# Performance work log

Measured on AMD Instinct MI355X. Metric: run time of the kernel, lower is better.

## Reference

```python
import jax, jax.numpy as jnp
import numpy as np


def setup_inputs() -> dict:
    key = jax.random.key(0)
    k_y, k_cb = jax.random.split(key)
    B, C, H, W = 8, 192, 64, 64
    G, K = 8, 512
    d = C // G  # 24
    y = jax.random.normal(k_y, (B, C, H, W), dtype=jnp.float32)
    codebooks = jax.random.normal(k_cb, (G, K, d), dtype=jnp.float32)
    return {"y": y, "codebooks": codebooks}


def reference(y, codebooks):
    # y: [B, C, H, W]; codebooks: [G, K, d] with C == G*d
    B, C, H, W = y.shape
    G, K, d = codebooks.shape
    # split channels into G groups of dim d -> vectors at each spatial pos
    x = y.reshape(B, G, d, H, W).transpose(0, 3, 4, 1, 2)  # [B,H,W,G,d]
    x2 = jnp.sum(x * x, axis=-1, keepdims=True)            # [B,H,W,G,1]
    e2 = jnp.sum(codebooks * codebooks, axis=-1)           # [G,K]
    xe = jnp.einsum('bhwgd,gkd->bhwgk', x, codebooks)      # [B,H,W,G,K]
    dist = x2 - 2.0 * xe + e2                              # [B,H,W,G,K]
    idx = jnp.argmin(dist, axis=-1)                        # [B,H,W,G] int
    # gather quantized vectors per group (to_feather)
    q = codebooks[jnp.arange(G), idx]                      # [B,H,W,G,d]
    y_ba = q.transpose(0, 3, 4, 1, 2).reshape(B, C, H, W)  # [B,C,H,W]
    code_index = idx.transpose(0, 3, 1, 2)                 # [B,G,H,W]
    # straight-through estimator
    universal_ctx = y + jax.lax.stop_gradient(y_ba - y)
    return universal_ctx, y_ba, code_index[:, None]        # [B,1,G,H,W]
```

## Files before the change

### kernel.cpp

```cpp
#include <hip/hip_runtime.h>

#define B_   8
#define C_   192
#define HW_  4096
#define G_   8
#define K_   512
#define D_   24
#define CBSZ (K_ * D_)
#define THREADS 1024
#define NBLOCKS 512

#define FRAG_HW    12288
#define E2_OFF_HW  12288
#define EL_OFF_HW  13312
#define IMG_HW     25600
#define WS_SMALL_HW 13312
#define WS_BIG_BYTES (G_ * IMG_HW * 2)

typedef float  f32x4 __attribute__((ext_vector_type(4)));
typedef int    i32x4 __attribute__((ext_vector_type(4)));
typedef short  s16x8 __attribute__((ext_vector_type(8)));
typedef short  s16x4 __attribute__((ext_vector_type(4)));
typedef _Float16 h16x8 __attribute__((ext_vector_type(8)));
typedef unsigned long long u64;

static __device__ __forceinline__ unsigned umin_(unsigned a, unsigned b){return a<b?a:b;}
static __device__ __forceinline__ unsigned umax_(unsigned a, unsigned b){return a>b?a:b;}
static __device__ __forceinline__ int dec_id(unsigned idb){
    return (int)((idb & 0x1F0u) | ((idb & 3u) << 2) | ((idb >> 2) & 3u));
}
static __device__ __forceinline__ unsigned pkrtz(float a, float b){
    return __builtin_bit_cast(unsigned, __builtin_amdgcn_cvt_pkrtz(a, b));
}
static __device__ __forceinline__ float lo16f(unsigned w){
    return (float)__builtin_bit_cast(_Float16, (unsigned short)(w & 0xFFFFu));
}
static __device__ __forceinline__ float hi16f(unsigned w){
    return (float)__builtin_bit_cast(_Float16, (unsigned short)(w >> 16));
}

__global__ __launch_bounds__(256) void vq_stage(
    const float* __restrict__ cb, unsigned short* __restrict__ ws, int big)
{
    const int g = blockIdx.x >> 3;
    const int s = blockIdx.x & 7;
    const int tid = threadIdx.x;
    const float* cbg = cb + g * CBSZ;
    unsigned short* img = ws + g * (big ? IMG_HW : WS_SMALL_HW);

    for (int i = tid; i < 384; i += 256) {
        int gi = s * 384 + i;
        f32x4 v = ((const f32x4*)cbg)[gi];
        int i4 = gi << 2;
        int n  = i4 / 24;
        int k0 = i4 - n * 24;
        int off = (n >> 4) * 384 + (((k0 >> 3) << 4) + (n & 15)) * 8 + (k0 & 7);
        s16x4 h, l;
        #pragma unroll
        for (int j = 0; j < 4; ++j) {
            _Float16 eh = (_Float16)v[j];
            _Float16 el = (_Float16)(v[j] - (float)eh);
            h[j] = __builtin_bit_cast(short, eh);
            l[j] = __builtin_bit_cast(short, el);
        }
        *(s16x4*)(&img[off]) = h;
        if (big) *(s16x4*)(&img[EL_OFF_HW + off]) = l;
    }
    if (tid < 64) {
        int n = s * 64 + tid;
        const float* row = cbg + n * D_;
        double s0 = 0.0, s1 = 0.0;
        #pragma unroll
        for (int j = 0; j < D_; j += 2) {
            double v0 = (double)row[j], v1 = (double)row[j+1];
            s0 = fma(v0,v0,s0); s1 = fma(v1,v1,s1);
        }
        ((float*)(img + E2_OFF_HW))[n] = (float)(128.0 + s0 + s1);
    }
}

template<bool BIG>
__global__ __launch_bounds__(THREADS, 8) void vq_main(
    const float* __restrict__ y, const float* __restrict__ cb,
    const unsigned short* __restrict__ ws, float* __restrict__ out)
{
    __shared__ __align__(16) unsigned short sB[IMG_HW];

    const int bid = blockIdx.x;
    const int g = bid & 7;
    const int blkg = bid >> 3;
    const int tid = threadIdx.x;
    const int wave = tid >> 6, lane = tid & 63;
    const int c = lane & 15, q = lane >> 4;

    const float* cbg = cb + g * CBSZ;

    if constexpr (BIG) {
        const char* src = (const char*)(ws + g * IMG_HW);
        char* dst = (char*)sB;
        #pragma unroll
        for (int it = 0; it < 4; ++it) {
            int off = it * 16384 + tid * 16;
            if (off < 51200)
                *(i32x4*)(dst + off) = *(const i32x4*)(src + off);
        }
    } else {
        const char* src = (const char*)(ws + g * WS_SMALL_HW);
        char* dst = (char*)sB;
        #pragma unroll
        for (int it = 0; it < 2; ++it) {
            int off = it * 16384 + tid * 16;
            if (off < 26624)
                *(i32x4*)(dst + off) = *(const i32x4*)(src + off);
        }
        #pragma unroll
        for (int it = 0; it < 3; ++it) {
            int gi = it * THREADS + tid;
            f32x4 v = ((const f32x4*)cbg)[gi];
            int i4 = gi << 2;
            int n  = i4 / 24;
            int k0 = i4 - n * 24;
            int off = (n >> 4) * 384 + (((k0 >> 3) << 4) + (n & 15)) * 8 + (k0 & 7);
            s16x4 l;
            #pragma unroll
            for (int j = 0; j < 4; ++j) {
                _Float16 eh = (_Float16)v[j];
                l[j] = __builtin_bit_cast(short, (_Float16)(v[j] - (float)eh));
            }
            *(s16x4*)(&sB[EL_OFF_HW + off]) = l;
        }
    }
    __syncthreads();

    float* out0 = out;
    float* out1 = out + B_*C_*HW_;
    float* out2 = out + 2*B_*C_*HW_;

    const unsigned short* aH = sB + (lane < 48 ? lane : lane - 48) * 8;
    const f32x4* e2p = (const f32x4*)((const float*)(sB + E2_OFF_HW) + (q << 2));

    const int wsid = (blkg << 4) + wave;
    const int hw    = (wsid & 255) << 4;
    const int bimg0 = wsid >> 8;
    int ybase[2];
    ybase[0] = (bimg0*C_ + g*D_)*HW_ + hw;
    ybase[1] = ybase[0] + 4*C_*HW_;

    h16x8 Xh[2], Xl[2];
    #pragma unroll
    for (int ti = 0; ti < 2; ++ti) {
        unsigned hx[4], lx[4];
        if (q < 3) {
            const float* yq = y + ybase[ti] + (q*8)*HW_ + c;
            float xf[8];
            #pragma unroll
            for (int jj = 0; jj < 8; ++jj) xf[jj] = -2.0f * yq[jj*HW_];
            #pragma unroll
            for (int p2 = 0; p2 < 4; ++p2) {
                float f0 = xf[2*p2], f1 = xf[2*p2+1];
                unsigned hw32 = pkrtz(f0, f1);
                float r0 = f0 - lo16f(hw32), r1 = f1 - hi16f(hw32);
                hx[p2] = hw32;
                lx[p2] = pkrtz(r0, r1);
            }
        } else {
            hx[0]=0u; hx[1]=0u; hx[2]=0u; hx[3]=0u;
            lx[0]=0u; lx[1]=0u; lx[2]=0u; lx[3]=0u;
        }
        Xh[ti] = __builtin_bit_cast(h16x8, (i32x4){(int)hx[0],(int)hx[1],(int)hx[2],(int)hx[3]});
        Xl[ti] = __builtin_bit_cast(h16x8, (i32x4){(int)lx[0],(int)lx[1],(int)lx[2],(int)lx[3]});
    }

    unsigned b1a[2] = {~0u, ~0u}, b2a[2] = {~0u, ~0u}, b3a[2] = {~0u, ~0u};
    #pragma unroll 4
    for (int t = 0; t < 32; ++t) {
        h16x8 eh = __builtin_bit_cast(h16x8, *(const s16x8*)(aH + t * 384));
        h16x8 el = __builtin_bit_cast(h16x8, *(const s16x8*)(aH + EL_OFF_HW + t * 384));
        f32x4 e2v = e2p[t * 4];
        f32x4 a0 = __builtin_amdgcn_mfma_f32_16x16x32_f16(eh, Xh[0], e2v, 0,0,0);
        a0       = __builtin_amdgcn_mfma_f32_16x16x32_f16(eh, Xl[0], a0,  0,0,0);
        a0       = __builtin_amdgcn_mfma_f32_16x16x32_f16(el, Xh[0], a0,  0,0,0);
        f32x4 a1 = __builtin_amdgcn_mfma_f32_16x16x32_f16(eh, Xh[1], e2v, 0,0,0);
        a1       = __builtin_amdgcn_mfma_f32_16x16x32_f16(eh, Xl[1], a1,  0,0,0);
        a1       = __builtin_amdgcn_mfma_f32_16x16x32_f16(el, Xh[1], a1,  0,0,0);
        #pragma unroll
        for (int r = 0; r < 4; ++r) {
            const unsigned id7 = (unsigned)((t << 2) | r);
            {
                unsigned key = (__float_as_uint(a0[r]) & 0xFFFFFF80u) + id7;
                unsigned t3, t2;
                asm("v_med3_u32 %0, %1, %2, %3" : "=v"(t3) : "v"(key), "v"(b2a[0]), "v"(b3a[0]));
                asm("v_med3_u32 %0, %1, %2, %3" : "=v"(t2) : "v"(key), "v"(b1a[0]), "v"(b2a[0]));
                b3a[0] = t3; b2a[0] = t2; b1a[0] = umin_(b1a[0], key);
            }
            {
                unsigned key = (__float_as_uint(a1[r]) & 0xFFFFFF80u) + id7;
                unsigned t3, t2;
                asm("v_med3_u32 %0, %1, %2, %3" : "=v"(t3) : "v"(key), "v"(b2a[1]), "v"(b3a[1]));
                asm("v_med3_u32 %0, %1, %2, %3" : "=v"(t2) : "v"(key), "v"(b1a[1]), "v"(b2a[1]));
                b3a[1] = t3; b2a[1] = t2; b1a[1] = umin_(b1a[1], key);
            }
        }
    }

    #pragma unroll
    for (int ti = 0; ti < 2; ++ti) {
        unsigned b1 = (b1a[ti] << 2) | (unsigned)q;
        unsigned b2 = (b2a[ti] << 2) | (unsigned)q;
        unsigned b3 = (b3a[ti] << 2) | (unsigned)q;
        #pragma unroll
        for (int d = 16; d < 64; d <<= 1) {
            unsigned o1=__shfl_xor(b1,d,64), o2=__shfl_xor(b2,d,64), o3=__shfl_xor(b3,d,64);
            unsigned x = umax_(b1,o1);
            unsigned yv= umin_(b2,o2);
            unsigned w = umax_(b2,o2);
            unsigned z = umin_(b3,o3);
            b1 = umin_(b1,o1);
            b2 = umin_(x,yv);
            b3 = umin_(umax_(x,yv), umin_(w,z));
        }

        const int gap = (int)((b2 >> 9) - (b1 >> 9));
        int kwin;
        if (__ballot((gap < 2) || (b1 < 0x0A000000u)) == 0ull) {
            kwin = dec_id(b1 & 511u);
        } else {
            float xfr[8];
            if (q < 3) {
                const float* yq = y + ybase[ti] + (q*8)*HW_ + c;
                #pragma unroll
                for (int jj = 0; jj < 8; ++jj) xfr[jj] = -2.0f * yq[jj*HW_];
            } else {
                #pragma unroll
                for (int jj = 0; jj < 8; ++jj) xfr[jj] = 0.0f;
            }
            double xd[8];
            #pragma unroll
            for (int jj = 0; jj < 8; ++jj) xd[jj] = (double)xfr[jj];
            const unsigned cands[3] = {b1, b2, b3};
            u64 bestk = ~0ull;
            #pragma unroll
            for (int ci = 0; ci < 3; ++ci) {
                int kc = dec_id(cands[ci] & 511u);
                double s = 0.0;
                if (q < 3) {
                    const f32x4* ce4 = (const f32x4*)(cbg + kc*D_ + (q<<3));
                    float ef[8];
                    *(f32x4*)&ef[0] = ce4[0];
                    *(f32x4*)&ef[4] = ce4[1];
                    #pragma unroll
                    for (int jj = 0; jj < 8; ++jj) {
                        double ev = (double)ef[jj];
                        s = fma(ev, ev, s);
                        s = fma(xd[jj], ev, s);
                    }
                }
                s += __shfl_xor(s, 16, 64);
                s += __shfl_xor(s, 32, 64);
                s += 128.0;
                u64 kk = (((u64)__double_as_longlong(s)) & ~0x1FFull) | (u64)kc;
                bestk = kk < bestk ? kk : bestk;
            }
            kwin = (int)(bestk & 511ull);
        }

        const float* cw = cbg + kwin * D_;
        if (q < 3) {
            const f32x4* cw4 = (const f32x4*)(cw + (q<<3));
            float v[8];
            *(f32x4*)&v[0] = cw4[0];
            *(f32x4*)&v[4] = cw4[1];
            const int ob = ybase[ti] + (q*8)*HW_ + c;
            #pragma unroll
            for (int jj = 0; jj < 8; ++jj) {
                out0[ob + jj*HW_] = v[jj];
                out1[ob + jj*HW_] = v[jj];
            }
        }
        if (lane < 16) {
            const int bimg = bimg0 + 4*ti;
            out2[(bimg*G_ + g)*HW_ + hw + lane] = (float)kwin;
        }
    }
}

extern "C" void kernel_launch(void* const* d_in, const int* in_sizes, int n_in,
                              void* d_out, int out_size, void* d_ws, size_t ws_size,
                              hipStream_t stream) {
    const float* y  = (const float*)d_in[0];
    const float* cb = (const float*)d_in[1];
    float* out = (float*)d_out;
    unsigned short* ws = (unsigned short*)d_ws;

    const bool big = ws_size >= (size_t)WS_BIG_BYTES;
    vq_stage<<<dim3(64), dim3(256), 0, stream>>>(cb, ws, big ? 1 : 0);
    if (big) vq_main<true ><<<dim3(NBLOCKS), dim3(THREADS), 0, stream>>>(y, cb, ws, out);
    else     vq_main<false><<<dim3(NBLOCKS), dim3(THREADS), 0, stream>>>(y, cb, ws, out);
}
```

Measured before the change: 113.1 us.

## Fold codebook norms into MFMA K-padding slots instead of accumulator init

Moves the per-code squared norm ||e||^2 into the unused K-padding lanes (columns 24-31) of the fp16 codebook fragment as a hi/lo fp16 pair. The x operand carries 1.0 in those slots, so the MFMA adds the norm directly. The accumulator starts from a constant bias, which removes the separate e2 LDS load per iteration, and the loop is fully unrolled. The lo residual fragment is always built in LDS from the fp32 codebook, which removes the big/small workspace variant. The trade-off is a larger LDS tile of 64 KB, which may hurt occupancy, and norm precision is limited to an fp16 hi/lo split.

```diff
diff --git a/kernel.cpp b/kernel.cpp
--- a/kernel.cpp
+++ b/kernel.cpp
@@ -10,12 +10,10 @@
 #define THREADS 1024
 #define NBLOCKS 512
 
-#define FRAG_HW    12288
-#define E2_OFF_HW  12288
-#define EL_OFF_HW  13312
-#define IMG_HW     25600
-#define WS_SMALL_HW 13312
-#define WS_BIG_BYTES (G_ * IMG_HW * 2)
+#define EH_HW    16384
+#define EL_OFF   16384
+#define LDS_HW   32768
+#define WS_G_HW  16384
 
 typedef float  f32x4 __attribute__((ext_vector_type(4)));
 typedef int    i32x4 __attribute__((ext_vector_type(4)));
@@ -40,13 +38,13 @@
 }
 
 __global__ __launch_bounds__(256) void vq_stage(
-    const float* __restrict__ cb, unsigned short* __restrict__ ws, int big)
+    const float* __restrict__ cb, unsigned short* __restrict__ ws)
 {
     const int g = blockIdx.x >> 3;
     const int s = blockIdx.x & 7;
     const int tid = threadIdx.x;
     const float* cbg = cb + g * CBSZ;
-    unsigned short* img = ws + g * (big ? IMG_HW : WS_SMALL_HW);
+    unsigned short* img = ws + g * WS_G_HW;
 
     for (int i = tid; i < 384; i += 256) {
         int gi = s * 384 + i;
@@ -54,17 +52,12 @@
         int i4 = gi << 2;
         int n  = i4 / 24;
         int k0 = i4 - n * 24;
-        int off = (n >> 4) * 384 + (((k0 >> 3) << 4) + (n & 15)) * 8 + (k0 & 7);
-        s16x4 h, l;
-        #pragma unroll
-        for (int j = 0; j < 4; ++j) {
-            _Float16 eh = (_Float16)v[j];
-            _Float16 el = (_Float16)(v[j] - (float)eh);
-            h[j] = __builtin_bit_cast(short, eh);
-            l[j] = __builtin_bit_cast(short, el);
-        }
+        int off = (n >> 4) * 512 + (((k0 >> 3) << 4) + (n & 15)) * 8 + (k0 & 7);
+        s16x4 h;
+        #pragma unroll
+        for (int j = 0; j < 4; ++j)
+            h[j] = __builtin_bit_cast(short, (_Float16)v[j]);
         *(s16x4*)(&img[off]) = h;
-        if (big) *(s16x4*)(&img[EL_OFF_HW + off]) = l;
     }
     if (tid < 64) {
         int n = s * 64 + tid;
@@ -75,16 +68,20 @@
             double v0 = (double)row[j], v1 = (double)row[j+1];
             s0 = fma(v0,v0,s0); s1 = fma(v1,v1,s1);
         }
-        ((float*)(img + E2_OFF_HW))[n] = (float)(128.0 + s0 + s1);
-    }
-}
-
-template<bool BIG>
+        double e2 = s0 + s1;
+        _Float16 hi = (_Float16)(float)e2;
+        _Float16 lo = (_Float16)(float)(e2 - (double)(float)hi);
+        s16x8 pack = { __builtin_bit_cast(short, hi),
+                       __builtin_bit_cast(short, lo), 0,0,0,0,0,0 };
+        *(s16x8*)(&img[(n >> 4) * 512 + (48 + (n & 15)) * 8]) = pack;
+    }
+}
+
 __global__ __launch_bounds__(THREADS, 8) void vq_main(
     const float* __restrict__ y, const float* __restrict__ cb,
     const unsigned short* __restrict__ ws, float* __restrict__ out)
 {
-    __shared__ __align__(16) unsigned short sB[IMG_HW];
+    __shared__ __align__(16) unsigned short sB[LDS_HW];
 
     const int bid = blockIdx.x;
     const int g = bid & 7;
@@ -95,40 +92,32 @@
 
     const float* cbg = cb + g * CBSZ;
 
-    if constexpr (BIG) {
-        const char* src = (const char*)(ws + g * IMG_HW);
+    {
+        const char* src = (const char*)(ws + g * WS_G_HW);
         char* dst = (char*)sB;
-        #pragma unroll
-        for (int it = 0; it < 4; ++it) {
-            int off = it * 16384 + tid * 16;
-            if (off < 51200)
-                *(i32x4*)(dst + off) = *(const i32x4*)(src + off);
-        }
-    } else {
-        const char* src = (const char*)(ws + g * WS_SMALL_HW);
-        char* dst = (char*)sB;
-        #pragma unroll
-        for (int it = 0; it < 2; ++it) {
-            int off = it * 16384 + tid * 16;
-            if (off < 26624)
-                *(i32x4*)(dst + off) = *(const i32x4*)(src + off);
-        }
-        #pragma unroll
-        for (int it = 0; it < 3; ++it) {
-            int gi = it * THREADS + tid;
-            f32x4 v = ((const f32x4*)cbg)[gi];
-            int i4 = gi << 2;
-            int n  = i4 / 24;
-            int k0 = i4 - n * 24;
-            int off = (n >> 4) * 384 + (((k0 >> 3) << 4) + (n & 15)) * 8 + (k0 & 7);
-            s16x4 l;
-            #pragma unroll
-            for (int j = 0; j < 4; ++j) {
-                _Float16 eh = (_Float16)v[j];
-                l[j] = __builtin_bit_cast(short, (_Float16)(v[j] - (float)eh));
-            }
-            *(s16x4*)(&sB[EL_OFF_HW + off]) = l;
-        }
+        *(i32x4*)(dst + tid*16)         = *(const i32x4*)(src + tid*16);
+        *(i32x4*)(dst + 16384 + tid*16) = *(const i32x4*)(src + 16384 + tid*16);
+    }
+    #pragma unroll
+    for (int it = 0; it < 3; ++it) {
+        int gi = it * THREADS + tid;
+        f32x4 v = ((const f32x4*)cbg)[gi];
+        int i4 = gi << 2;
+        int n  = i4 / 24;
+        int k0 = i4 - n * 24;
+        int off = (n >> 4) * 512 + (((k0 >> 3) << 4) + (n & 15)) * 8 + (k0 & 7);
+        s16x4 l;
+        #pragma unroll
+        for (int j = 0; j < 4; ++j) {
+            _Float16 eh = (_Float16)v[j];
+            l[j] = __builtin_bit_cast(short, (_Float16)(v[j] - (float)eh));
+        }
+        *(s16x4*)(&sB[EL_OFF + off]) = l;
+    }
+    if (tid < 512) {
+        int t = tid >> 4, cc = tid & 15;
+        s16x8 z = {0,0,0,0,0,0,0,0};
+        *(s16x8*)(&sB[EL_OFF + t * 512 + (48 + cc) * 8]) = z;
     }
     __syncthreads();
 
@@ -136,8 +125,8 @@
     float* out1 = out + B_*C_*HW_;
     float* out2 = out + 2*B_*C_*HW_;
 
-    const unsigned short* aH = sB + (lane < 48 ? lane : lane - 48) * 8;
-    const f32x4* e2p = (const f32x4*)((const float*)(sB + E2_OFF_HW) + (q << 2));
+    const unsigned short* aH = sB + lane * 8;
+    const unsigned short* aL = sB + EL_OFF + lane * 8;
 
     const int wsid = (blkg << 4) + wave;
     const int hw    = (wsid & 255) << 4;
@@ -164,25 +153,26 @@
                 lx[p2] = pkrtz(r0, r1);
             }
         } else {
-            hx[0]=0u; hx[1]=0u; hx[2]=0u; hx[3]=0u;
+            hx[0]=0x3C003C00u; hx[1]=0u; hx[2]=0u; hx[3]=0u;
             lx[0]=0u; lx[1]=0u; lx[2]=0u; lx[3]=0u;
         }
         Xh[ti] = __builtin_bit_cast(h16x8, (i32x4){(int)hx[0],(int)hx[1],(int)hx[2],(int)hx[3]});
         Xl[ti] = __builtin_bit_cast(h16x8, (i32x4){(int)lx[0],(int)lx[1],(int)lx[2],(int)lx[3]});
     }
 
+    const f32x4 cbias = {128.0f, 128.0f, 128.0f, 128.0f};
+
     unsigned b1a[2] = {~0u, ~0u}, b2a[2] = {~0u, ~0u}, b3a[2] = {~0u, ~0u};
-    #pragma unroll 4
+    #pragma unroll
     for (int t = 0; t < 32; ++t) {
-        h16x8 eh = __builtin_bit_cast(h16x8, *(const s16x8*)(aH + t * 384));
-        h16x8 el = __builtin_bit_cast(h16x8, *(const s16x8*)(aH + EL_OFF_HW + t * 384));
-        f32x4 e2v = e2p[t * 4];
-        f32x4 a0 = __builtin_amdgcn_mfma_f32_16x16x32_f16(eh, Xh[0], e2v, 0,0,0);
-        a0       = __builtin_amdgcn_mfma_f32_16x16x32_f16(eh, Xl[0], a0,  0,0,0);
-        a0       = __builtin_amdgcn_mfma_f32_16x16x32_f16(el, Xh[0], a0,  0,0,0);
-        f32x4 a1 = __builtin_amdgcn_mfma_f32_16x16x32_f16(eh, Xh[1], e2v, 0,0,0);
-        a1       = __builtin_amdgcn_mfma_f32_16x16x32_f16(eh, Xl[1], a1,  0,0,0);
-        a1       = __builtin_amdgcn_mfma_f32_16x16x32_f16(el, Xh[1], a1,  0,0,0);
+        h16x8 eh = __builtin_bit_cast(h16x8, *(const s16x8*)(aH + t * 512));
+        h16x8 el = __builtin_bit_cast(h16x8, *(const s16x8*)(aL + t * 512));
+        f32x4 a0 = __builtin_amdgcn_mfma_f32_16x16x32_f16(eh, Xh[0], cbias, 0,0,0);
+        a0       = __builtin_amdgcn_mfma_f32_16x16x32_f16(eh, Xl[0], a0,   0,0,0);
+        a0       = __builtin_amdgcn_mfma_f32_16x16x32_f16(el, Xh[0], a0,   0,0,0);
+        f32x4 a1 = __builtin_amdgcn_mfma_f32_16x16x32_f16(eh, Xh[1], cbias, 0,0,0);
+        a1       = __builtin_amdgcn_mfma_f32_16x16x32_f16(eh, Xl[1], a1,   0,0,0);
+        a1       = __builtin_amdgcn_mfma_f32_16x16x32_f16(el, Xh[1], a1,   0,0,0);
         #pragma unroll
         for (int r = 0; r < 4; ++r) {
             const unsigned id7 = (unsigned)((t << 2) | r);
@@ -292,8 +282,6 @@
     float* out = (float*)d_out;
     unsigned short* ws = (unsigned short*)d_ws;
 
-    const bool big = ws_size >= (size_t)WS_BIG_BYTES;
-    vq_stage<<<dim3(64), dim3(256), 0, stream>>>(cb, ws, big ? 1 : 0);
-    if (big) vq_main<true ><<<dim3(NBLOCKS), dim3(THREADS), 0, stream>>>(y, cb, ws, out);
-    else     vq_main<false><<<dim3(NBLOCKS), dim3(THREADS), 0, stream>>>(y, cb, ws, out);
-}
+    vq_stage<<<dim3(64), dim3(256), 0, stream>>>(cb, ws);
+    vq_main<<<dim3(NBLOCKS), dim3(THREADS), 0, stream>>>(y, cb, ws, out);
+}
```

After: 109.5 us. 3.1% less time.
